# Optimization experiments

Hardware: AMD Instinct MI355X
Metric: run time of the kernel (lower is better)

The kernel has to match this reference:

```python
import jax, jax.numpy as jnp
import numpy as np

LAMBDA = 0.01  # sparsity_threshold
SCALE = 0.02
NUM_BLOCKS = 4


def setup_inputs() -> dict:
    key = jax.random.key(0)
    k1, k2, k3, k4, k5 = jax.random.split(key, 5)
    B, N, C = 8, 4096, 512
    bs = C // NUM_BLOCKS
    return {
        "x": jax.random.normal(k1, (B, N, C), dtype=jnp.float32),
        "w1": jax.random.normal(k2, (2, NUM_BLOCKS, bs, bs), dtype=jnp.float32) * SCALE,
        "w2": jax.random.normal(k3, (2, NUM_BLOCKS, bs, bs), dtype=jnp.float32) * SCALE,
        "b1": jax.random.normal(k4, (2, NUM_BLOCKS, bs), dtype=jnp.float32) * SCALE,
        "b2": jax.random.normal(k5, (2, NUM_BLOCKS, bs), dtype=jnp.float32) * SCALE,
        "H": 64,
        "W": 64,
    }


def _softshrink(v):
    return jnp.where(v > LAMBDA, v - LAMBDA, jnp.where(v < -LAMBDA, v + LAMBDA, jnp.zeros((), v.dtype)))


def reference(x, w1, w2, b1, b2, H, W):
    B, N, C = x.shape
    bs = C // NUM_BLOCKS
    xb = x.reshape(B, N, NUM_BLOCKS, bs)
    # FFT over (token, block) axes, ortho norm — faithful to torch fft2(dim=(1,2))
    xf = jnp.fft.fft2(xb, axes=(1, 2), norm="ortho")
    re, im = jnp.real(xf), jnp.imag(xf)

    mul = lambda a, w: jnp.einsum("tnbd,bdk->tnbk", a, w)  # block-diagonal matmul

    r1 = jax.nn.relu(mul(re, w1[0]) - mul(im, w1[1]) + b1[0])
    i1 = jax.nn.relu(mul(re, w1[1]) + mul(im, w1[0]) + b1[1])
    r2 = mul(r1, w2[0]) - mul(i1, w2[1]) + b2[0]
    i2 = mul(r1, w2[1]) + mul(i1, w2[0]) + b2[1]

    z = _softshrink(r2) + 1j * _softshrink(i2)
    out = jnp.real(jnp.fft.ifft2(z, axes=(1, 2), norm="ortho"))  # .to(float32) keeps real part
    return out.reshape(B, N, C).astype(jnp.float32)
```

## Files before the change

kernel.cpp:

```cpp
#include <hip/hip_runtime.h>
#include <math.h>

#define TWO_PI 6.283185307179586f

typedef __attribute__((ext_vector_type(8))) short bf16x8;
typedef __attribute__((ext_vector_type(4))) short bf16x4;
typedef __attribute__((ext_vector_type(4))) float f32x4;
typedef __attribute__((ext_vector_type(4))) _Float16 h16x4;
typedef __attribute__((ext_vector_type(8))) _Float16 h16x8;

__device__ __forceinline__ short f2bf(float f) {
    unsigned u = __float_as_uint(f);
    unsigned r = (u + 0x7FFFu + ((u >> 16) & 1u)) >> 16;
    return (short)r;
}
__device__ __forceinline__ float bf2f(short s) {
    return __uint_as_float(((unsigned)(unsigned short)s) << 16);
}

__device__ __forceinline__ int dr4(int s) {
    return ((s & 3) << 4) | (s & 12) | ((s >> 4) & 3);
}

__device__ __forceinline__ void cmulw(float& xr, float& xi, float wr, float wi) {
    const float tr = xr * wr - xi * wi;
    xi = xr * wi + xi * wr;
    xr = tr;
}

__device__ __forceinline__ f32x4 ld4bf(const char* Z, int off) {
    const bf16x4 v = *(const bf16x4*)(Z + off);
    f32x4 r;
    r[0] = bf2f(v[0]); r[1] = bf2f(v[1]); r[2] = bf2f(v[2]); r[3] = bf2f(v[3]);
    return r;
}
__device__ __forceinline__ void st4bf(char* Z, int off, f32x4 a) {
    bf16x4 v;
    v[0] = f2bf(a[0]); v[1] = f2bf(a[1]); v[2] = f2bf(a[2]); v[3] = f2bf(a[3]);
    *(bf16x4*)(Z + off) = v;
}

__device__ __forceinline__ int swzoff(int r, int cb) {
    return r * 256 + (cb ^ ((r & 7) << 4));
}

__device__ __forceinline__ void dif_stage_bf(char* Z, const float* wtr, const float* wti,
                                             int cb, int h, int s) {
    const int q  = 16 >> (2 * s);
    const int tw = 1 << (2 * s);
    const int j = h & (q - 1);
    const int g = (s == 0) ? 0 : (h >> (4 - 2 * s));
    const int i0 = g * (q << 2) + j;
    const int i1 = i0 + q, i2 = i1 + q, i3 = i2 + q;
    const int o0 = swzoff(i0, cb), o1 = swzoff(i1, cb);
    const int o2 = swzoff(i2, cb), o3 = swzoff(i3, cb);
    const f32x4 a0r = ld4bf(Z, o0), a0i = ld4bf(Z + 16384, o0);
    const f32x4 a1r = ld4bf(Z, o1), a1i = ld4bf(Z + 16384, o1);
    const f32x4 a2r = ld4bf(Z, o2), a2i = ld4bf(Z + 16384, o2);
    const f32x4 a3r = ld4bf(Z, o3), a3i = ld4bf(Z + 16384, o3);
    const int m = j * tw;
    const float w1r = wtr[m],     w1i = wti[m];
    const float w2r = wtr[2 * m], w2i = wti[2 * m];
    const float w3r = wtr[3 * m], w3i = wti[3 * m];
    f32x4 O0r, O0i, O1r, O1i, O2r, O2i, O3r, O3i;
#pragma unroll
    for (int e = 0; e < 4; ++e) {
        const float t0r = a0r[e] + a2r[e], t0i = a0i[e] + a2i[e];
        const float t2r = a0r[e] - a2r[e], t2i = a0i[e] - a2i[e];
        const float t1r = a1r[e] + a3r[e], t1i = a1i[e] + a3i[e];
        const float dr  = a1r[e] - a3r[e], di  = a1i[e] - a3i[e];
        const float t3r = di, t3i = -dr;
        O0r[e] = t0r + t1r;  O0i[e] = t0i + t1i;
        float y1r = t2r + t3r, y1i = t2i + t3i;
        float y2r = t0r - t1r, y2i = t0i - t1i;
        float y3r = t2r - t3r, y3i = t2i - t3i;
        if (m) {
            cmulw(y1r, y1i, w1r, w1i);
            cmulw(y2r, y2i, w2r, w2i);
            cmulw(y3r, y3i, w3r, w3i);
        }
        O1r[e] = y1r; O1i[e] = y1i;
        O2r[e] = y2r; O2i[e] = y2i;
        O3r[e] = y3r; O3i[e] = y3i;
    }
    st4bf(Z, o0, O0r);  st4bf(Z + 16384, o0, O0i);
    st4bf(Z, o1, O1r);  st4bf(Z + 16384, o1, O1i);
    st4bf(Z, o2, O2r);  st4bf(Z + 16384, o2, O2i);
    st4bf(Z, o3, O3r);  st4bf(Z + 16384, o3, O3i);
}

__device__ __forceinline__ void dit_stage_bf(char* Z, const float* wtr, const float* wti,
                                             int cb, int h, int s) {
    const int q  = 16 >> (2 * s);
    const int tw = 1 << (2 * s);
    const int j = h & (q - 1);
    const int g = (s == 0) ? 0 : (h >> (4 - 2 * s));
    const int i0 = g * (q << 2) + j;
    const int i1 = i0 + q, i2 = i1 + q, i3 = i2 + q;
    const int o0 = swzoff(i0, cb), o1 = swzoff(i1, cb);
    const int o2 = swzoff(i2, cb), o3 = swzoff(i3, cb);
    const f32x4 a0r = ld4bf(Z, o0), a0i = ld4bf(Z + 16384, o0);
    const f32x4 a1r = ld4bf(Z, o1), a1i = ld4bf(Z + 16384, o1);
    const f32x4 a2r = ld4bf(Z, o2), a2i = ld4bf(Z + 16384, o2);
    const f32x4 a3r = ld4bf(Z, o3), a3i = ld4bf(Z + 16384, o3);
    const int m = j * tw;
    const float w1r = wtr[m],     w1i = -wti[m];
    const float w2r = wtr[2 * m], w2i = -wti[2 * m];
    const float w3r = wtr[3 * m], w3i = -wti[3 * m];
    f32x4 O0r, O0i, O1r, O1i, O2r, O2i, O3r, O3i;
#pragma unroll
    for (int e = 0; e < 4; ++e) {
        float b1r = a1r[e], b1i = a1i[e];
        float b2r = a2r[e], b2i = a2i[e];
        float b3r = a3r[e], b3i = a3i[e];
        if (m) {
            cmulw(b1r, b1i, w1r, w1i);
            cmulw(b2r, b2i, w2r, w2i);
            cmulw(b3r, b3i, w3r, w3i);
        }
        const float u0r = a0r[e] + b2r, u0i = a0i[e] + b2i;
        const float u1r = a0r[e] - b2r, u1i = a0i[e] - b2i;
        const float u2r = b1r + b3r,    u2i = b1i + b3i;
        const float dr  = b1r - b3r,    di  = b1i - b3i;
        const float u3r = -di, u3i = dr;
        O0r[e] = u0r + u2r; O0i[e] = u0i + u2i;
        O1r[e] = u1r + u3r; O1i[e] = u1i + u3i;
        O2r[e] = u0r - u2r; O2i[e] = u0i - u2i;
        O3r[e] = u1r - u3r; O3i[e] = u1i - u3i;
    }
    st4bf(Z, o0, O0r);  st4bf(Z + 16384, o0, O0i);
    st4bf(Z, o1, O1r);  st4bf(Z + 16384, o1, O1i);
    st4bf(Z, o2, O2r);  st4bf(Z + 16384, o2, O2i);
    st4bf(Z, o3, O3r);  st4bf(Z + 16384, o3, O3i);
}

__device__ __forceinline__ void stage_ztile(const short* __restrict__ zre,
                                            const short* __restrict__ zim,
                                            char* Zbuf, int b, int dg, int ct,
                                            int wave, int lane) {
#pragma unroll
    for (int it = 0; it < 4; ++it) {
        const int q = wave * 256 + it * 64 + lane;
        const int p = q >> 10;
        const int r = q & 1023;
        const int slot = r >> 4;
        const int c = r & 15;
        const int c_log = c ^ (slot & 7);
        const int blk = c_log >> 2, cj = c_log & 3;
        const short* src = p ? zim : zre;
        const size_t g = ((size_t)(b * 4096 + dg * 64 + slot) * 512)
                       + (size_t)(blk * 128 + ct * 32 + cj * 8);
        unsigned* lp = (unsigned*)(Zbuf + (wave * 4096 + it * 1024));
        __builtin_amdgcn_global_load_lds((const unsigned*)(src + g), lp, 16, 0, 0);
    }
}

#define DECODE_BCT() \
    const int b  = blockIdx.x >> 8; \
    const int dg = (blockIdx.x >> 2) & 63; \
    const int ct = blockIdx.x & 3;

#define GADDR(slot, blk, f4) \
    (((size_t)(b * 4096 + (slot)) * 512) + (size_t)((blk) * 128 + ct * 32 + (f4) * 4))

#define GADDR8(slot, blk, e8) \
    (((size_t)(b * 4096 + (slot)) * 512) + (size_t)((blk) * 128 + ct * 32 + (e8) * 8))

#define SETUP_TABLE48() \
    if (tid < 48) { \
        float s_, c_; \
        sincosf(TWO_PI * (float)tid / 64.0f, &s_, &c_); \
        wre[tid] = c_; wim[tid] = -s_; \
    }

extern "C" __global__ void __launch_bounds__(512)
fft_fwd_a(const float* __restrict__ x, short* __restrict__ zre, short* __restrict__ zim) {
    __shared__ __align__(16) _Float16 Lre[64][136];
    __shared__ __align__(16) _Float16 Lim[64][136];
    __shared__ float wre[48], wim[48];
    __shared__ float twr[64], twi[64];
    const int tid = threadIdx.x;
    SETUP_TABLE48();
    DECODE_BCT();
    if (tid >= 64 && tid < 128) {
        const int s1 = tid - 64;
        float sn, cs;
        sincosf(-(TWO_PI / 4096.0f) * (float)(dg * dr4(s1)), &sn, &cs);
        twr[s1] = cs; twi[s1] = sn;
    }
    for (int idx = tid; idx < 2048; idx += 512) {
        const int n1 = idx >> 5, q = idx & 31, blk = q >> 3, f4 = q & 7;
        const int cl = blk * 32 + f4 * 4;
        const float4 v = *(const float4*)(x + GADDR(n1 * 64 + dg, blk, f4));
        h16x4 hv, hz;
        hv[0] = (_Float16)v.x; hv[1] = (_Float16)v.y;
        hv[2] = (_Float16)v.z; hv[3] = (_Float16)v.w;
        hz[0] = (_Float16)0.f; hz[1] = (_Float16)0.f;
        hz[2] = (_Float16)0.f; hz[3] = (_Float16)0.f;
        *(h16x4*)&Lre[n1][cl] = hv;
        *(h16x4*)&Lim[n1][cl] = hz;
    }
    {
        const int c4 = (tid & 31) * 4;
        const int h = tid >> 5;
#pragma unroll
        for (int s = 0; s < 3; ++s) {
            const int q  = 16 >> (2 * s);
            const int tw = 1 << (2 * s);
            __syncthreads();
            const int j = h & (q - 1);
            const int g = (s == 0) ? 0 : (h >> (4 - 2 * s));
            const int i0 = g * (q << 2) + j;
            const int i1 = i0 + q, i2 = i1 + q, i3 = i2 + q;
            const h16x4 A0r = *(const h16x4*)&Lre[i0][c4], A0i = *(const h16x4*)&Lim[i0][c4];
            const h16x4 A1r = *(const h16x4*)&Lre[i1][c4], A1i = *(const h16x4*)&Lim[i1][c4];
            const h16x4 A2r = *(const h16x4*)&Lre[i2][c4], A2i = *(const h16x4*)&Lim[i2][c4];
            const h16x4 A3r = *(const h16x4*)&Lre[i3][c4], A3i = *(const h16x4*)&Lim[i3][c4];
            const int m = j * tw;
            const float w1r = wre[m],     w1i = wim[m];
            const float w2r = wre[2 * m], w2i = wim[2 * m];
            const float w3r = wre[3 * m], w3i = wim[3 * m];
            h16x4 O0r, O0i, O1r, O1i, O2r, O2i, O3r, O3i;
#pragma unroll
            for (int e = 0; e < 4; ++e) {
                const float a0r = (float)A0r[e], a0i = (float)A0i[e];
                const float a1r = (float)A1r[e], a1i = (float)A1i[e];
                const float a2r = (float)A2r[e], a2i = (float)A2i[e];
                const float a3r = (float)A3r[e], a3i = (float)A3i[e];
                const float t0r = a0r + a2r, t0i = a0i + a2i;
                const float t2r = a0r - a2r, t2i = a0i - a2i;
                const float t1r = a1r + a3r, t1i = a1i + a3i;
                const float dr  = a1r - a3r, di  = a1i - a3i;
                const float t3r = di, t3i = -dr;
                O0r[e] = (_Float16)(t0r + t1r);  O0i[e] = (_Float16)(t0i + t1i);
                float y1r = t2r + t3r, y1i = t2i + t3i;
                float y2r = t0r - t1r, y2i = t0i - t1i;
                float y3r = t2r - t3r, y3i = t2i - t3i;
                if (m) {
                    cmulw(y1r, y1i, w1r, w1i);
                    cmulw(y2r, y2i, w2r, w2i);
                    cmulw(y3r, y3i, w3r, w3i);
                }
                O1r[e] = (_Float16)y1r; O1i[e] = (_Float16)y1i;
                O2r[e] = (_Float16)y2r; O2i[e] = (_Float16)y2i;
                O3r[e] = (_Float16)y3r; O3i[e] = (_Float16)y3i;
            }
            *(h16x4*)&Lre[i0][c4] = O0r;  *(h16x4*)&Lim[i0][c4] = O0i;
            *(h16x4*)&Lre[i1][c4] = O1r;  *(h16x4*)&Lim[i1][c4] = O1i;
            *(h16x4*)&Lre[i2][c4] = O2r;  *(h16x4*)&Lim[i2][c4] = O2i;
            *(h16x4*)&Lre[i3][c4] = O3r;  *(h16x4*)&Lim[i3][c4] = O3i;
        }
        __syncthreads();
    }
    for (int idx = tid; idx < 2048; idx += 512) {
        const int s1 = idx >> 5, q = idx & 31, blk = q >> 3, f4 = q & 7;
        const int cl = blk * 32 + f4 * 4;
        const float cs = twr[s1], sn = twi[s1];
        const h16x4 hr = *(const h16x4*)&Lre[s1][cl];
        const h16x4 hi = *(const h16x4*)&Lim[s1][cl];
        bf16x4 pr, pi;
#pragma unroll
        for (int i = 0; i < 4; ++i) {
            const float vr = (float)hr[i], vi = (float)hi[i];
            pr[i] = f2bf(vr * cs - vi * sn);
            pi[i] = f2bf(vr * sn + vi * cs);
        }
        const size_t g = GADDR(s1 * 64 + dg, blk, f4);
        *(bf16x4*)(zre + g) = pr;
        *(bf16x4*)(zim + g) = pi;
    }
}

extern "C" __global__ void __launch_bounds__(512)
fft_fwd_b(short* __restrict__ zre, short* __restrict__ zim) {
    __shared__ __align__(16) char Zs[2][32768];
    __shared__ float wre[48], wim[48];
    const int tid = threadIdx.x;
    SETUP_TABLE48();
    const int bh = blockIdx.x >> 8;
    const int dg = (blockIdx.x >> 2) & 63;
    const int ct = blockIdx.x & 3;
    const int wave = tid >> 6, lane = tid & 63;
    const int cb = (tid & 31) * 8;
    const int h  = tid >> 5;

    stage_ztile(zre, zim, Zs[0], bh * 4, dg, ct, wave, lane);

    for (int t = 0; t < 4; ++t) {
        __syncthreads();
        if (t + 1 < 4)
            stage_ztile(zre, zim, Zs[(t + 1) & 1], bh * 4 + t + 1, dg, ct, wave, lane);

        char* Z = Zs[t & 1];
        dif_stage_bf(Z, wre, wim, cb, h, 0);
        __syncthreads();
        dif_stage_bf(Z, wre, wim, cb, h, 1);
        __syncthreads();
        dif_stage_bf(Z, wre, wim, cb, h, 2);
        __syncthreads();

        {
            const int slot = tid >> 3, jg4 = tid & 7;
            const int jb = jg4 * 8;
            f32x4 r[4], m[4];
#pragma unroll
            for (int b4 = 0; b4 < 4; ++b4) {
                const int off = swzoff(slot, b4 * 64 + jb);
                r[b4] = ld4bf(Z, off);
                m[b4] = ld4bf(Z + 16384, off);
            }
            const float sc = 1.0f / 128.0f;
            f32x4 yr[4], ym[4];
#pragma unroll
            for (int e = 0; e < 4; ++e) {
                const float r0 = r[0][e], r1 = r[1][e], r2 = r[2][e], r3 = r[3][e];
                const float m0 = m[0][e], m1 = m[1][e], m2 = m[2][e], m3 = m[3][e];
                yr[0][e] = (r0 + r1 + r2 + r3) * sc;  ym[0][e] = (m0 + m1 + m2 + m3) * sc;
                yr[1][e] = (r0 + m1 - r2 - m3) * sc;  ym[1][e] = (m0 - r1 - m2 + r3) * sc;
                yr[2][e] = (r0 - r1 + r2 - r3) * sc;  ym[2][e] = (m0 - m1 + m2 - m3) * sc;
                yr[3][e] = (r0 - m1 - r2 + m3) * sc;  ym[3][e] = (m0 + r1 - m2 - r3) * sc;
            }
#pragma unroll
            for (int b4 = 0; b4 < 4; ++b4) {
                const int off = swzoff(slot, b4 * 64 + jb);
                st4bf(Z, off, yr[b4]);
                st4bf(Z + 16384, off, ym[b4]);
            }
        }
        __syncthreads();

        const int b = bh * 4 + t;
#pragma unroll
        for (int kq = 0; kq < 4; ++kq) {
            const int q = wave * 256 + kq * 64 + lane;
            const int p = q >> 10;
            const int r2 = q & 1023;
            const int slot = r2 >> 4;
            const int c = r2 & 15;
            const int c_log = c ^ (slot & 7);
            const int blk = c_log >> 2, cj = c_log & 3;
            const bf16x8 v = *(const bf16x8*)(Z + q * 16);
            short* dst = p ? zim : zre;
            const size_t g = ((size_t)(b * 4096 + dg * 64 + slot) * 512)
                           + (size_t)(blk * 128 + ct * 32 + cj * 8);
            *(bf16x8*)(dst + g) = v;
        }
    }
}

extern "C" __global__ void __launch_bounds__(512)
fft_inv_a(short* __restrict__ zre, short* __restrict__ zim) {
    __shared__ __align__(16) char Zs[2][32768];
    __shared__ float wre[48], wim[48];
    __shared__ float twr[64], twi[64];
    const int tid = threadIdx.x;
    SETUP_TABLE48();
    const int bh = blockIdx.x >> 8;
    const int dg = (blockIdx.x >> 2) & 63;
    const int ct = blockIdx.x & 3;
    if (tid >= 64 && tid < 128) {
        const int n2 = tid - 64;
        float sn, cs;
        sincosf((TWO_PI / 4096.0f) * (float)(n2 * dr4(dg)), &sn, &cs);
        twr[n2] = cs; twi[n2] = sn;
    }
    const int wave = tid >> 6, lane = tid & 63;
    const int cb = (tid & 31) * 8;
    const int h  = tid >> 5;

    stage_ztile(zre, zim, Zs[0], bh * 4, dg, ct, wave, lane);

    for (int t = 0; t < 4; ++t) {
        __syncthreads();
        if (t + 1 < 4)
            stage_ztile(zre, zim, Zs[(t + 1) & 1], bh * 4 + t + 1, dg, ct, wave, lane);

        char* Z = Zs[t & 1];

        {
            const int slot = tid >> 3, jg4 = tid & 7;
            const int jb = jg4 * 8;
            f32x4 r[4], m[4];
#pragma unroll
            for (int b4 = 0; b4 < 4; ++b4) {
                const int off = swzoff(slot, b4 * 64 + jb);
                r[b4] = ld4bf(Z, off);
                m[b4] = ld4bf(Z + 16384, off);
            }
            const float sc = 1.0f / 128.0f;
            f32x4 yr[4], ym[4];
#pragma unroll
            for (int e = 0; e < 4; ++e) {
                const float r0 = r[0][e], r1 = r[1][e], r2 = r[2][e], r3 = r[3][e];
                const float m0 = m[0][e], m1 = m[1][e], m2 = m[2][e], m3 = m[3][e];
                yr[0][e] = (r0 + r1 + r2 + r3) * sc;  ym[0][e] = (m0 + m1 + m2 + m3) * sc;
                yr[1][e] = (r0 - m1 - r2 + m3) * sc;  ym[1][e] = (m0 + r1 - m2 - r3) * sc;
                yr[2][e] = (r0 - r1 + r2 - r3) * sc;  ym[2][e] = (m0 - m1 + m2 - m3) * sc;
                yr[3][e] = (r0 + m1 - r2 - m3) * sc;  ym[3][e] = (m0 - r1 - m2 + r3) * sc;
            }
#pragma unroll
            for (int b4 = 0; b4 < 4; ++b4) {
                const int off = swzoff(slot, b4 * 64 + jb);
                st4bf(Z, off, yr[b4]);
                st4bf(Z + 16384, off, ym[b4]);
            }
        }
        __syncthreads();
        dit_stage_bf(Z, wre, wim, cb, h, 2);
        __syncthreads();
        dit_stage_bf(Z, wre, wim, cb, h, 1);
        __syncthreads();
        dit_stage_bf(Z, wre, wim, cb, h, 0);
        __syncthreads();

        const int b = bh * 4 + t;
#pragma unroll
        for (int k = 0; k < 2; ++k) {
            const int idx = tid + k * 512;
            const int slot = idx >> 4;
            const int c = idx & 15;
            const int c_log = c ^ (slot & 7);
            const int blk = c_log >> 2, cj = c_log & 3;
            const bf16x8 vr = *(const bf16x8*)(Z + slot * 256 + c * 16);
            const bf16x8 vi = *(const bf16x8*)(Z + 16384 + slot * 256 + c * 16);
            const float cs = twr[slot], sn = twi[slot];
            bf16x8 pr, pi;
#pragma unroll
            for (int i = 0; i < 8; ++i) {
                const float ar = bf2f(vr[i]), ai = bf2f(vi[i]);
                pr[i] = f2bf(ar * cs - ai * sn);
                pi[i] = f2bf(ar * sn + ai * cs);
            }
            const size_t g = ((size_t)(b * 4096 + dg * 64 + slot) * 512)
                           + (size_t)(blk * 128 + ct * 32 + cj * 8);
            *(bf16x8*)(zre + g) = pr;
            *(bf16x8*)(zim + g) = pi;
        }
    }
}

extern "C" __global__ void __launch_bounds__(512)
fft_inv_b(const short* __restrict__ zre, const short* __restrict__ zim,
          float* __restrict__ out) {
    __shared__ __align__(16) _Float16 Lre[64][136];
    __shared__ __align__(16) _Float16 Lim[64][136];
    __shared__ float wre[48], wim[48];
    const int tid = threadIdx.x;
    SETUP_TABLE48();
    DECODE_BCT();
    for (int idx = tid; idx < 1024; idx += 512) {
        const int s1 = idx >> 4, q = idx & 15, blk = q >> 2, e8 = q & 3;
        const int cl = blk * 32 + e8 * 8;
        const size_t g = GADDR8(s1 * 64 + dg, blk, e8);
        const bf16x8 vr = *(const bf16x8*)(zre + g);
        const bf16x8 vi = *(const bf16x8*)(zim + g);
        h16x8 hr, hi;
#pragma unroll
        for (int i = 0; i < 8; ++i) {
            hr[i] = (_Float16)bf2f(vr[i]);
            hi[i] = (_Float16)bf2f(vi[i]);
        }
        *(h16x8*)&Lre[s1][cl] = hr;
        *(h16x8*)&Lim[s1][cl] = hi;
    }
    {
        const int c4 = (tid & 31) * 4;
        const int h = tid >> 5;
#pragma unroll
        for (int s = 2; s >= 0; --s) {
            const int q  = 16 >> (2 * s);
            const int tw = 1 << (2 * s);
            __syncthreads();
            const int j = h & (q - 1);
            const int g = (s == 0) ? 0 : (h >> (4 - 2 * s));
            const int i0 = g * (q << 2) + j;
            const int i1 = i0 + q, i2 = i1 + q, i3 = i2 + q;
            const h16x4 A0r = *(const h16x4*)&Lre[i0][c4], A0i = *(const h16x4*)&Lim[i0][c4];
            const h16x4 A1r = *(const h16x4*)&Lre[i1][c4], A1i = *(const h16x4*)&Lim[i1][c4];
            const h16x4 A2r = *(const h16x4*)&Lre[i2][c4], A2i = *(const h16x4*)&Lim[i2][c4];
            const h16x4 A3r = *(const h16x4*)&Lre[i3][c4], A3i = *(const h16x4*)&Lim[i3][c4];
            const int m = j * tw;
            const float w1r = wre[m],     w1i = -wim[m];
            const float w2r = wre[2 * m], w2i = -wim[2 * m];
            const float w3r = wre[3 * m], w3i = -wim[3 * m];
            h16x4 O0r, O0i, O1r, O1i, O2r, O2i, O3r, O3i;
#pragma unroll
            for (int e = 0; e < 4; ++e) {
                float b1r = (float)A1r[e], b1i = (float)A1i[e];
                float b2r = (float)A2r[e], b2i = (float)A2i[e];
                float b3r = (float)A3r[e], b3i = (float)A3i[e];
                if (m) {
                    cmulw(b1r, b1i, w1r, w1i);
                    cmulw(b2r, b2i, w2r, w2i);
                    cmulw(b3r, b3i, w3r, w3i);
                }
                const float a0r = (float)A0r[e], a0i = (float)A0i[e];
                const float u0r = a0r + b2r, u0i = a0i + b2i;
                const float u1r = a0r - b2r, u1i = a0i - b2i;
                const float u2r = b1r + b3r, u2i = b1i + b3i;
                const float dr  = b1r - b3r, di  = b1i - b3i;
                const float u3r = -di, u3i = dr;
                O0r[e] = (_Float16)(u0r + u2r); O0i[e] = (_Float16)(u0i + u2i);
                O1r[e] = (_Float16)(u1r + u3r); O1i[e] = (_Float16)(u1i + u3i);
                O2r[e] = (_Float16)(u0r - u2r); O2i[e] = (_Float16)(u0i - u2i);
                O3r[e] = (_Float16)(u1r - u3r); O3i[e] = (_Float16)(u1i - u3i);
            }
            *(h16x4*)&Lre[i0][c4] = O0r;  *(h16x4*)&Lim[i0][c4] = O0i;
            *(h16x4*)&Lre[i1][c4] = O1r;  *(h16x4*)&Lim[i1][c4] = O1i;
            *(h16x4*)&Lre[i2][c4] = O2r;  *(h16x4*)&Lim[i2][c4] = O2i;
            *(h16x4*)&Lre[i3][c4] = O3r;  *(h16x4*)&Lim[i3][c4] = O3i;
        }
        __syncthreads();
    }
    for (int idx = tid; idx < 2048; idx += 512) {
        const int n1 = idx >> 5, q = idx & 31, blk = q >> 3, f4 = q & 7;
        const int cl = blk * 32 + f4 * 4;
        const h16x4 hr = *(const h16x4*)&Lre[n1][cl];
        float4 o;
        o.x = (float)hr[0]; o.y = (float)hr[1];
        o.z = (float)hr[2]; o.w = (float)hr[3];
        *(float4*)(out + GADDR(n1 * 64 + dg, blk, f4)) = o;
    }
}

extern "C" __global__ void __launch_bounds__(256)
wprep(const float* __restrict__ w1, const float* __restrict__ w2,
      short* __restrict__ wb) {
    const int i4  = blockIdx.x * 256 + threadIdx.x;
    const int k0  = (i4 & 63) * 4;
    const int n   = (i4 >> 6) & 255;
    const int blk = (i4 >> 14) & 3;
    const int L   = i4 >> 16;
    const float* w = L ? w2 : w1;
    bf16x4 pv;
#pragma unroll
    for (int j = 0; j < 4; ++j) {
        const int k = k0 + j;
        float v;
        if (k < 128) {
            v = (n < 128) ? w[blk * 16384 + k * 128 + n]
                          : w[65536 + blk * 16384 + k * 128 + (n - 128)];
        } else {
            v = (n < 128) ? -w[65536 + blk * 16384 + (k - 128) * 128 + n]
                          :  w[blk * 16384 + (k - 128) * 128 + (n - 128)];
        }
        pv[j] = f2bf(v);
    }
    *(bf16x4*)(wb + (size_t)i4 * 4) = pv;
}

#define MITER 4

__device__ __forceinline__ void stage_tile(const short* __restrict__ zre,
                                           const short* __restrict__ zim,
                                           char* Abuf, int rowbase, int blk,
                                           int wave, int lane) {
#pragma unroll
    for (int it = 0; it < 4; ++it) {
        const int chunk = wave * 256 + it * 64 + lane;
        const int row   = chunk >> 5;
        const unsigned kbyte = ((unsigned)((chunk & 31) << 4)) ^ ((unsigned)((row & 7) << 4));
        const int k0 = (int)(kbyte >> 1);
        const short* src = (k0 < 128) ? zre : zim;
        const size_t g = (size_t)(rowbase + row) * 512 + blk * 128 + (k0 & 127);
        unsigned* lp = (unsigned*)(Abuf + (wave * 4096 + it * 1024));
        __builtin_amdgcn_global_load_lds((const unsigned*)(src + g), lp, 16, 0, 0);
    }
}

template<int LAYER>
__global__ void __launch_bounds__(512)
mlp_mfma(short* __restrict__ zre, short* __restrict__ zim,
         const short* __restrict__ wb, const float* __restrict__ bias) {
    __shared__ __align__(16) char As[2][64 * 256 * 2];

    const int blk  = blockIdx.y;
    const int tid  = threadIdx.x;
    const int wave = tid >> 6;
    const int lane = tid & 63;
    const int lrow = lane & 15;
    const int lk   = lane >> 4;

    bf16x8 Bf[2][8];
#pragma unroll
    for (int nt = 0; nt < 2; ++nt) {
        const int n = wave * 32 + nt * 16 + lrow;
#pragma unroll
        for (int ks = 0; ks < 8; ++ks) {
            Bf[nt][ks] = *(const bf16x8*)(wb + ((size_t)(blk * 256 + n) * 256 + ks * 32 + lk * 8));
        }
    }

    float bv[2];
#pragma unroll
    for (int nt = 0; nt < 2; ++nt) {
        const int n = wave * 32 + nt * 16 + lrow;
        bv[nt] = (n < 128) ? bias[blk * 128 + n] : bias[512 + blk * 128 + (n - 128)];
    }

    stage_tile(zre, zim, As[0], blockIdx.x * MITER * 64, blk, wave, lane);

    for (int t = 0; t < MITER; ++t) {
        __syncthreads();

        if (t + 1 < MITER)
            stage_tile(zre, zim, As[(t + 1) & 1],
                       (blockIdx.x * MITER + t + 1) * 64, blk, wave, lane);

        const char* Ab = As[t & 1];
        const int rowbase = (blockIdx.x * MITER + t) * 64;

        f32x4 acc[4][2];
#pragma unroll
        for (int mt = 0; mt < 4; ++mt)
#pragma unroll
            for (int nt = 0; nt < 2; ++nt)
                acc[mt][nt] = (f32x4){0.f, 0.f, 0.f, 0.f};

#pragma unroll
        for (int ks = 0; ks < 8; ++ks) {
            bf16x8 af[4];
#pragma unroll
            for (int mt = 0; mt < 4; ++mt) {
                const int row = mt * 16 + lrow;
                const int k0  = ks * 32 + lk * 8;
                const unsigned byteoff =
                    ((unsigned)(row * 512 + k0 * 2)) ^ ((unsigned)((row & 7) << 4));
                af[mt] = *(const bf16x8*)(Ab + byteoff);
            }
#pragma unroll
            for (int mt = 0; mt < 4; ++mt)
#pragma unroll
                for (int nt = 0; nt < 2; ++nt)
                    acc[mt][nt] = __builtin_amdgcn_mfma_f32_16x16x32_bf16(
                        af[mt], Bf[nt][ks], acc[mt][nt], 0, 0, 0);
        }

#pragma unroll
        for (int nt = 0; nt < 2; ++nt) {
            const int n = wave * 32 + nt * 16 + lrow;
            short* dst = (n < 128) ? zre : zim;
            const int col = blk * 128 + (n & 127);
#pragma unroll
            for (int mt = 0; mt < 4; ++mt) {
#pragma unroll
                for (int r = 0; r < 4; ++r) {
                    const int row = rowbase + mt * 16 + lk * 4 + r;
                    float v = acc[mt][nt][r] + bv[nt];
                    if (LAYER == 1) {
                        v = fmaxf(v, 0.0f);
                    } else {
                        v = (v > 0.01f) ? v - 0.01f : ((v < -0.01f) ? v + 0.01f : 0.0f);
                    }
                    dst[(size_t)row * 512 + col] = f2bf(v);
                }
            }
        }
    }
}

extern "C" void kernel_launch(void* const* d_in, const int* in_sizes, int n_in,
                              void* d_out, int out_size, void* d_ws, size_t ws_size,
                              hipStream_t stream) {
    const float* x  = (const float*)d_in[0];
    const float* w1 = (const float*)d_in[1];
    const float* w2 = (const float*)d_in[2];
    const float* b1 = (const float*)d_in[3];
    const float* b2 = (const float*)d_in[4];

    float* out = (float*)d_out;
    short* zre = (short*)d_ws;
    short* zim = zre + 16777216;
    short* wb  = (short*)d_out;
    const size_t WB_L = 4ull * 256 * 256;

    wprep<<<512, 256, 0, stream>>>(w1, w2, wb);

    fft_fwd_a<<<2048, 512, 0, stream>>>(x, zre, zim);
    fft_fwd_b<<<512, 512, 0, stream>>>(zre, zim);

    mlp_mfma<1><<<dim3(32768 / (64 * MITER), 4), 512, 0, stream>>>(zre, zim, wb, b1);
    mlp_mfma<2><<<dim3(32768 / (64 * MITER), 4), 512, 0, stream>>>(zre, zim, wb + WB_L, b2);

    fft_inv_a<<<512, 512, 0, stream>>>(zre, zim);
    fft_inv_b<<<2048, 512, 0, stream>>>(zre, zim, out);
}
```

Before: 235.3 us.

## Move 4-point block DFT into token-FFT kernels and halve per-block batch loop

The radix-4 DFT over the channel-block axis moves out of fft_fwd_b and fft_inv_a. It now runs in registers at the end of fft_fwd_a (after the twiddle) and at the start of fft_inv_b, which removes one LDS read/write pass and a barrier from each of the heavy 64x64 kernels. fft_fwd_b and fft_inv_a drop their double-buffered LDS staging for a single buffer and process two batches per block instead of four, with twice as many blocks launched. Results are read into registers before the next tile is staged. The radix-4 64-point butterflies are factored into shared templates. The trade-off is less load/compute overlap inside each block, in exchange for lower LDS use and more blocks in flight.

```diff
diff --git a/kernel.cpp b/kernel.cpp
--- a/kernel.cpp
+++ b/kernel.cpp
@@ -163,15 +163,117 @@
 #define GADDR(slot, blk, f4) \
     (((size_t)(b * 4096 + (slot)) * 512) + (size_t)((blk) * 128 + ct * 32 + (f4) * 4))
 
-#define GADDR8(slot, blk, e8) \
-    (((size_t)(b * 4096 + (slot)) * 512) + (size_t)((blk) * 128 + ct * 32 + (e8) * 8))
-
 #define SETUP_TABLE48() \
     if (tid < 48) { \
         float s_, c_; \
         sincosf(TWO_PI * (float)tid / 64.0f, &s_, &c_); \
         wre[tid] = c_; wim[tid] = -s_; \
     }
+
+template<int W>
+__device__ __forceinline__ void fft64_dif4v(_Float16 (*Lre)[W], _Float16 (*Lim)[W],
+                                            const float* wtr, const float* wti,
+                                            int c4, int h) {
+#pragma unroll
+    for (int s = 0; s < 3; ++s) {
+        const int q  = 16 >> (2 * s);
+        const int tw = 1 << (2 * s);
+        __syncthreads();
+        const int j = h & (q - 1);
+        const int g = (s == 0) ? 0 : (h >> (4 - 2 * s));
+        const int i0 = g * (q << 2) + j;
+        const int i1 = i0 + q, i2 = i1 + q, i3 = i2 + q;
+        const h16x4 A0r = *(const h16x4*)&Lre[i0][c4], A0i = *(const h16x4*)&Lim[i0][c4];
+        const h16x4 A1r = *(const h16x4*)&Lre[i1][c4], A1i = *(const h16x4*)&Lim[i1][c4];
+        const h16x4 A2r = *(const h16x4*)&Lre[i2][c4], A2i = *(const h16x4*)&Lim[i2][c4];
+        const h16x4 A3r = *(const h16x4*)&Lre[i3][c4], A3i = *(const h16x4*)&Lim[i3][c4];
+        const int m = j * tw;
+        const float w1r = wtr[m],     w1i = wti[m];
+        const float w2r = wtr[2 * m], w2i = wti[2 * m];
+        const float w3r = wtr[3 * m], w3i = wti[3 * m];
+        h16x4 O0r, O0i, O1r, O1i, O2r, O2i, O3r, O3i;
+#pragma unroll
+        for (int e = 0; e < 4; ++e) {
+            const float a0r = (float)A0r[e], a0i = (float)A0i[e];
+            const float a1r = (float)A1r[e], a1i = (float)A1i[e];
+            const float a2r = (float)A2r[e], a2i = (float)A2i[e];
+            const float a3r = (float)A3r[e], a3i = (float)A3i[e];
+            const float t0r = a0r + a2r, t0i = a0i + a2i;
+            const float t2r = a0r - a2r, t2i = a0i - a2i;
+            const float t1r = a1r + a3r, t1i = a1i + a3i;
+            const float dr  = a1r - a3r, di  = a1i - a3i;
+            const float t3r = di, t3i = -dr;
+            O0r[e] = (_Float16)(t0r + t1r);  O0i[e] = (_Float16)(t0i + t1i);
+            float y1r = t2r + t3r, y1i = t2i + t3i;
+            float y2r = t0r - t1r, y2i = t0i - t1i;
+            float y3r = t2r - t3r, y3i = t2i - t3i;
+            if (m) {
+                cmulw(y1r, y1i, w1r, w1i);
+                cmulw(y2r, y2i, w2r, w2i);
+                cmulw(y3r, y3i, w3r, w3i);
+            }
+            O1r[e] = (_Float16)y1r; O1i[e] = (_Float16)y1i;
+            O2r[e] = (_Float16)y2r; O2i[e] = (_Float16)y2i;
+            O3r[e] = (_Float16)y3r; O3i[e] = (_Float16)y3i;
+        }
+        *(h16x4*)&Lre[i0][c4] = O0r;  *(h16x4*)&Lim[i0][c4] = O0i;
+        *(h16x4*)&Lre[i1][c4] = O1r;  *(h16x4*)&Lim[i1][c4] = O1i;
+        *(h16x4*)&Lre[i2][c4] = O2r;  *(h16x4*)&Lim[i2][c4] = O2i;
+        *(h16x4*)&Lre[i3][c4] = O3r;  *(h16x4*)&Lim[i3][c4] = O3i;
+    }
+    __syncthreads();
+}
+
+template<int W>
+__device__ __forceinline__ void fft64_dit4v(_Float16 (*Lre)[W], _Float16 (*Lim)[W],
+                                            const float* wtr, const float* wti,
+                                            int c4, int h) {
+#pragma unroll
+    for (int s = 2; s >= 0; --s) {
+        const int q  = 16 >> (2 * s);
+        const int tw = 1 << (2 * s);
+        __syncthreads();
+        const int j = h & (q - 1);
+        const int g = (s == 0) ? 0 : (h >> (4 - 2 * s));
+        const int i0 = g * (q << 2) + j;
+        const int i1 = i0 + q, i2 = i1 + q, i3 = i2 + q;
+        const h16x4 A0r = *(const h16x4*)&Lre[i0][c4], A0i = *(const h16x4*)&Lim[i0][c4];
+        const h16x4 A1r = *(const h16x4*)&Lre[i1][c4], A1i = *(const h16x4*)&Lim[i1][c4];
+        const h16x4 A2r = *(const h16x4*)&Lre[i2][c4], A2i = *(const h16x4*)&Lim[i2][c4];
+        const h16x4 A3r = *(const h16x4*)&Lre[i3][c4], A3i = *(const h16x4*)&Lim[i3][c4];
+        const int m = j * tw;
+        const float w1r = wtr[m],     w1i = -wti[m];
+        const float w2r = wtr[2 * m], w2i = -wti[2 * m];
+        const float w3r = wtr[3 * m], w3i = -wti[3 * m];
+        h16x4 O0r, O0i, O1r, O1i, O2r, O2i, O3r, O3i;
+#pragma unroll
+        for (int e = 0; e < 4; ++e) {
+            float b1r = (float)A1r[e], b1i = (float)A1i[e];
+            float b2r = (float)A2r[e], b2i = (float)A2i[e];
+            float b3r = (float)A3r[e], b3i = (float)A3i[e];
+            if (m) {
+                cmulw(b1r, b1i, w1r, w1i);
+                cmulw(b2r, b2i, w2r, w2i);
+                cmulw(b3r, b3i, w3r, w3i);
+            }
+            const float a0r = (float)A0r[e], a0i = (float)A0i[e];
+            const float u0r = a0r + b2r, u0i = a0i + b2i;
+            const float u1r = a0r - b2r, u1i = a0i - b2i;
+            const float u2r = b1r + b3r, u2i = b1i + b3i;
+            const float dr  = b1r - b3r, di  = b1i - b3i;
+            const float u3r = -di, u3i = dr;
+            O0r[e] = (_Float16)(u0r + u2r); O0i[e] = (_Float16)(u0i + u2i);
+            O1r[e] = (_Float16)(u1r + u3r); O1i[e] = (_Float16)(u1i + u3i);
+            O2r[e] = (_Float16)(u0r - u2r); O2i[e] = (_Float16)(u0i - u2i);
+            O3r[e] = (_Float16)(u1r - u3r); O3i[e] = (_Float16)(u1i - u3i);
+        }
+        *(h16x4*)&Lre[i0][c4] = O0r;  *(h16x4*)&Lim[i0][c4] = O0i;
+        *(h16x4*)&Lre[i1][c4] = O1r;  *(h16x4*)&Lim[i1][c4] = O1i;
+        *(h16x4*)&Lre[i2][c4] = O2r;  *(h16x4*)&Lim[i2][c4] = O2i;
+        *(h16x4*)&Lre[i3][c4] = O3r;  *(h16x4*)&Lim[i3][c4] = O3i;
+    }
+    __syncthreads();
+}
 
 extern "C" __global__ void __launch_bounds__(512)
 fft_fwd_a(const float* __restrict__ x, short* __restrict__ zre, short* __restrict__ zim) {
@@ -200,80 +302,52 @@
         *(h16x4*)&Lre[n1][cl] = hv;
         *(h16x4*)&Lim[n1][cl] = hz;
     }
+    fft64_dif4v<136>(Lre, Lim, wre, wim, (tid & 31) * 4, tid >> 5);
     {
-        const int c4 = (tid & 31) * 4;
-        const int h = tid >> 5;
-#pragma unroll
-        for (int s = 0; s < 3; ++s) {
-            const int q  = 16 >> (2 * s);
-            const int tw = 1 << (2 * s);
-            __syncthreads();
-            const int j = h & (q - 1);
-            const int g = (s == 0) ? 0 : (h >> (4 - 2 * s));
-            const int i0 = g * (q << 2) + j;
-            const int i1 = i0 + q, i2 = i1 + q, i3 = i2 + q;
-            const h16x4 A0r = *(const h16x4*)&Lre[i0][c4], A0i = *(const h16x4*)&Lim[i0][c4];
-            const h16x4 A1r = *(const h16x4*)&Lre[i1][c4], A1i = *(const h16x4*)&Lim[i1][c4];
-            const h16x4 A2r = *(const h16x4*)&Lre[i2][c4], A2i = *(const h16x4*)&Lim[i2][c4];
-            const h16x4 A3r = *(const h16x4*)&Lre[i3][c4], A3i = *(const h16x4*)&Lim[i3][c4];
-            const int m = j * tw;
-            const float w1r = wre[m],     w1i = wim[m];
-            const float w2r = wre[2 * m], w2i = wim[2 * m];
-            const float w3r = wre[3 * m], w3i = wim[3 * m];
-            h16x4 O0r, O0i, O1r, O1i, O2r, O2i, O3r, O3i;
+        const int s1 = tid >> 3, f4 = tid & 7;
+        const float cs = twr[s1], sn = twi[s1];
+        f32x4 r[4], m[4];
+#pragma unroll
+        for (int blk = 0; blk < 4; ++blk) {
+            const int cl = blk * 32 + f4 * 4;
+            const h16x4 hr = *(const h16x4*)&Lre[s1][cl];
+            const h16x4 hi = *(const h16x4*)&Lim[s1][cl];
 #pragma unroll
             for (int e = 0; e < 4; ++e) {
-                const float a0r = (float)A0r[e], a0i = (float)A0i[e];
-                const float a1r = (float)A1r[e], a1i = (float)A1i[e];
-                const float a2r = (float)A2r[e], a2i = (float)A2i[e];
-                const float a3r = (float)A3r[e], a3i = (float)A3i[e];
-                const float t0r = a0r + a2r, t0i = a0i + a2i;
-                const float t2r = a0r - a2r, t2i = a0i - a2i;
-                const float t1r = a1r + a3r, t1i = a1i + a3i;
-                const float dr  = a1r - a3r, di  = a1i - a3i;
-                const float t3r = di, t3i = -dr;
-                O0r[e] = (_Float16)(t0r + t1r);  O0i[e] = (_Float16)(t0i + t1i);
-                float y1r = t2r + t3r, y1i = t2i + t3i;
-                float y2r = t0r - t1r, y2i = t0i - t1i;
-                float y3r = t2r - t3r, y3i = t2i - t3i;
-                if (m) {
-                    cmulw(y1r, y1i, w1r, w1i);
-                    cmulw(y2r, y2i, w2r, w2i);
-                    cmulw(y3r, y3i, w3r, w3i);
-                }
-                O1r[e] = (_Float16)y1r; O1i[e] = (_Float16)y1i;
-                O2r[e] = (_Float16)y2r; O2i[e] = (_Float16)y2i;
-                O3r[e] = (_Float16)y3r; O3i[e] = (_Float16)y3i;
-            }
-            *(h16x4*)&Lre[i0][c4] = O0r;  *(h16x4*)&Lim[i0][c4] = O0i;
-            *(h16x4*)&Lre[i1][c4] = O1r;  *(h16x4*)&Lim[i1][c4] = O1i;
-            *(h16x4*)&Lre[i2][c4] = O2r;  *(h16x4*)&Lim[i2][c4] = O2i;
-            *(h16x4*)&Lre[i3][c4] = O3r;  *(h16x4*)&Lim[i3][c4] = O3i;
-        }
-        __syncthreads();
-    }
-    for (int idx = tid; idx < 2048; idx += 512) {
-        const int s1 = idx >> 5, q = idx & 31, blk = q >> 3, f4 = q & 7;
-        const int cl = blk * 32 + f4 * 4;
-        const float cs = twr[s1], sn = twi[s1];
-        const h16x4 hr = *(const h16x4*)&Lre[s1][cl];
-        const h16x4 hi = *(const h16x4*)&Lim[s1][cl];
-        bf16x4 pr, pi;
-#pragma unroll
-        for (int i = 0; i < 4; ++i) {
-            const float vr = (float)hr[i], vi = (float)hi[i];
-            pr[i] = f2bf(vr * cs - vi * sn);
-            pi[i] = f2bf(vr * sn + vi * cs);
-        }
-        const size_t g = GADDR(s1 * 64 + dg, blk, f4);
-        *(bf16x4*)(zre + g) = pr;
-        *(bf16x4*)(zim + g) = pi;
+                const float vr = (float)hr[e], vi = (float)hi[e];
+                r[blk][e] = vr * cs - vi * sn;
+                m[blk][e] = vr * sn + vi * cs;
+            }
+        }
+        const float sc = 1.0f / 128.0f;
+        f32x4 yr[4], ym[4];
+#pragma unroll
+        for (int e = 0; e < 4; ++e) {
+            const float r0 = r[0][e], r1 = r[1][e], r2 = r[2][e], r3 = r[3][e];
+            const float m0 = m[0][e], m1 = m[1][e], m2 = m[2][e], m3 = m[3][e];
+            yr[0][e] = (r0 + r1 + r2 + r3) * sc;  ym[0][e] = (m0 + m1 + m2 + m3) * sc;
+            yr[1][e] = (r0 + m1 - r2 - m3) * sc;  ym[1][e] = (m0 - r1 - m2 + r3) * sc;
+            yr[2][e] = (r0 - r1 + r2 - r3) * sc;  ym[2][e] = (m0 - m1 + m2 - m3) * sc;
+            yr[3][e] = (r0 - m1 - r2 + m3) * sc;  ym[3][e] = (m0 + r1 - m2 - r3) * sc;
+        }
+#pragma unroll
+        for (int blk = 0; blk < 4; ++blk) {
+            bf16x4 pr, pi;
+#pragma unroll
+            for (int e = 0; e < 4; ++e) {
+                pr[e] = f2bf(yr[blk][e]);
+                pi[e] = f2bf(ym[blk][e]);
+            }
+            const size_t g = GADDR(s1 * 64 + dg, blk, f4);
+            *(bf16x4*)(zre + g) = pr;
+            *(bf16x4*)(zim + g) = pi;
+        }
     }
 }
 
 extern "C" __global__ void __launch_bounds__(512)
 fft_fwd_b(short* __restrict__ zre, short* __restrict__ zim) {
-    __shared__ __align__(16) char Zs[2][32768];
+    __shared__ __align__(16) char Zs[32768];
     __shared__ float wre[48], wim[48];
     const int tid = threadIdx.x;
     SETUP_TABLE48();
@@ -284,52 +358,26 @@
     const int cb = (tid & 31) * 8;
     const int h  = tid >> 5;
 
-    stage_ztile(zre, zim, Zs[0], bh * 4, dg, ct, wave, lane);
-
-    for (int t = 0; t < 4; ++t) {
-        __syncthreads();
-        if (t + 1 < 4)
-            stage_ztile(zre, zim, Zs[(t + 1) & 1], bh * 4 + t + 1, dg, ct, wave, lane);
-
-        char* Z = Zs[t & 1];
-        dif_stage_bf(Z, wre, wim, cb, h, 0);
-        __syncthreads();
-        dif_stage_bf(Z, wre, wim, cb, h, 1);
-        __syncthreads();
-        dif_stage_bf(Z, wre, wim, cb, h, 2);
-        __syncthreads();
-
-        {
-            const int slot = tid >> 3, jg4 = tid & 7;
-            const int jb = jg4 * 8;
-            f32x4 r[4], m[4];
-#pragma unroll
-            for (int b4 = 0; b4 < 4; ++b4) {
-                const int off = swzoff(slot, b4 * 64 + jb);
-                r[b4] = ld4bf(Z, off);
-                m[b4] = ld4bf(Z + 16384, off);
-            }
-            const float sc = 1.0f / 128.0f;
-            f32x4 yr[4], ym[4];
-#pragma unroll
-            for (int e = 0; e < 4; ++e) {
-                const float r0 = r[0][e], r1 = r[1][e], r2 = r[2][e], r3 = r[3][e];
-                const float m0 = m[0][e], m1 = m[1][e], m2 = m[2][e], m3 = m[3][e];
-                yr[0][e] = (r0 + r1 + r2 + r3) * sc;  ym[0][e] = (m0 + m1 + m2 + m3) * sc;
-                yr[1][e] = (r0 + m1 - r2 - m3) * sc;  ym[1][e] = (m0 - r1 - m2 + r3) * sc;
-                yr[2][e] = (r0 - r1 + r2 - r3) * sc;  ym[2][e] = (m0 - m1 + m2 - m3) * sc;
-                yr[3][e] = (r0 - m1 - r2 + m3) * sc;  ym[3][e] = (m0 + r1 - m2 - r3) * sc;
-            }
-#pragma unroll
-            for (int b4 = 0; b4 < 4; ++b4) {
-                const int off = swzoff(slot, b4 * 64 + jb);
-                st4bf(Z, off, yr[b4]);
-                st4bf(Z + 16384, off, ym[b4]);
-            }
-        }
-        __syncthreads();
-
-        const int b = bh * 4 + t;
+    stage_ztile(zre, zim, Zs, bh * 2, dg, ct, wave, lane);
+
+    for (int t = 0; t < 2; ++t) {
+        __syncthreads();
+        dif_stage_bf(Zs, wre, wim, cb, h, 0);
+        __syncthreads();
+        dif_stage_bf(Zs, wre, wim, cb, h, 1);
+        __syncthreads();
+        dif_stage_bf(Zs, wre, wim, cb, h, 2);
+        __syncthreads();
+        bf16x8 vout[4];
+#pragma unroll
+        for (int kq = 0; kq < 4; ++kq) {
+            const int q = wave * 256 + kq * 64 + lane;
+            vout[kq] = *(const bf16x8*)(Zs + q * 16);
+        }
+        __syncthreads();
+        if (t + 1 < 2)
+            stage_ztile(zre, zim, Zs, bh * 2 + t + 1, dg, ct, wave, lane);
+        const int b = bh * 2 + t;
 #pragma unroll
         for (int kq = 0; kq < 4; ++kq) {
             const int q = wave * 256 + kq * 64 + lane;
@@ -339,18 +387,17 @@
             const int c = r2 & 15;
             const int c_log = c ^ (slot & 7);
             const int blk = c_log >> 2, cj = c_log & 3;
-            const bf16x8 v = *(const bf16x8*)(Z + q * 16);
             short* dst = p ? zim : zre;
             const size_t g = ((size_t)(b * 4096 + dg * 64 + slot) * 512)
                            + (size_t)(blk * 128 + ct * 32 + cj * 8);
-            *(bf16x8*)(dst + g) = v;
+            *(bf16x8*)(dst + g) = vout[kq];
         }
     }
 }
 
 extern "C" __global__ void __launch_bounds__(512)
 fft_inv_a(short* __restrict__ zre, short* __restrict__ zim) {
-    __shared__ __align__(16) char Zs[2][32768];
+    __shared__ __align__(16) char Zs[32768];
     __shared__ float wre[48], wim[48];
     __shared__ float twr[64], twi[64];
     const int tid = threadIdx.x;
@@ -368,52 +415,36 @@
     const int cb = (tid & 31) * 8;
     const int h  = tid >> 5;
 
-    stage_ztile(zre, zim, Zs[0], bh * 4, dg, ct, wave, lane);
-
-    for (int t = 0; t < 4; ++t) {
-        __syncthreads();
-        if (t + 1 < 4)
-            stage_ztile(zre, zim, Zs[(t + 1) & 1], bh * 4 + t + 1, dg, ct, wave, lane);
-
-        char* Z = Zs[t & 1];
-
-        {
-            const int slot = tid >> 3, jg4 = tid & 7;
-            const int jb = jg4 * 8;
-            f32x4 r[4], m[4];
-#pragma unroll
-            for (int b4 = 0; b4 < 4; ++b4) {
-                const int off = swzoff(slot, b4 * 64 + jb);
-                r[b4] = ld4bf(Z, off);
-                m[b4] = ld4bf(Z + 16384, off);
-            }
-            const float sc = 1.0f / 128.0f;
-            f32x4 yr[4], ym[4];
-#pragma unroll
-            for (int e = 0; e < 4; ++e) {
-                const float r0 = r[0][e], r1 = r[1][e], r2 = r[2][e], r3 = r[3][e];
-                const float m0 = m[0][e], m1 = m[1][e], m2 = m[2][e], m3 = m[3][e];
-                yr[0][e] = (r0 + r1 + r2 + r3) * sc;  ym[0][e] = (m0 + m1 + m2 + m3) * sc;
-                yr[1][e] = (r0 - m1 - r2 + m3) * sc;  ym[1][e] = (m0 + r1 - m2 - r3) * sc;
-                yr[2][e] = (r0 - r1 + r2 - r3) * sc;  ym[2][e] = (m0 - m1 + m2 - m3) * sc;
-                yr[3][e] = (r0 + m1 - r2 - m3) * sc;  ym[3][e] = (m0 - r1 - m2 + r3) * sc;
-            }
-#pragma unroll
-            for (int b4 = 0; b4 < 4; ++b4) {
-                const int off = swzoff(slot, b4 * 64 + jb);
-                st4bf(Z, off, yr[b4]);
-                st4bf(Z + 16384, off, ym[b4]);
-            }
-        }
-        __syncthreads();
-        dit_stage_bf(Z, wre, wim, cb, h, 2);
-        __syncthreads();
-        dit_stage_bf(Z, wre, wim, cb, h, 1);
-        __syncthreads();
-        dit_stage_bf(Z, wre, wim, cb, h, 0);
-        __syncthreads();
-
-        const int b = bh * 4 + t;
+    stage_ztile(zre, zim, Zs, bh * 2, dg, ct, wave, lane);
+
+    for (int t = 0; t < 2; ++t) {
+        __syncthreads();
+        dit_stage_bf(Zs, wre, wim, cb, h, 2);
+        __syncthreads();
+        dit_stage_bf(Zs, wre, wim, cb, h, 1);
+        __syncthreads();
+        dit_stage_bf(Zs, wre, wim, cb, h, 0);
+        __syncthreads();
+        bf16x8 pr[2], pi[2];
+#pragma unroll
+        for (int k = 0; k < 2; ++k) {
+            const int idx = tid + k * 512;
+            const int slot = idx >> 4;
+            const int c = idx & 15;
+            const bf16x8 vr = *(const bf16x8*)(Zs + slot * 256 + c * 16);
+            const bf16x8 vi = *(const bf16x8*)(Zs + 16384 + slot * 256 + c * 16);
+            const float cs = twr[slot], sn = twi[slot];
+#pragma unroll
+            for (int i = 0; i < 8; ++i) {
+                const float ar = bf2f(vr[i]), ai = bf2f(vi[i]);
+                pr[k][i] = f2bf(ar * cs - ai * sn);
+                pi[k][i] = f2bf(ar * sn + ai * cs);
+            }
+        }
+        __syncthreads();
+        if (t + 1 < 2)
+            stage_ztile(zre, zim, Zs, bh * 2 + t + 1, dg, ct, wave, lane);
+        const int b = bh * 2 + t;
 #pragma unroll
         for (int k = 0; k < 2; ++k) {
             const int idx = tid + k * 512;
@@ -421,20 +452,10 @@
             const int c = idx & 15;
             const int c_log = c ^ (slot & 7);
             const int blk = c_log >> 2, cj = c_log & 3;
-            const bf16x8 vr = *(const bf16x8*)(Z + slot * 256 + c * 16);
-            const bf16x8 vi = *(const bf16x8*)(Z + 16384 + slot * 256 + c * 16);
-            const float cs = twr[slot], sn = twi[slot];
-            bf16x8 pr, pi;
-#pragma unroll
-            for (int i = 0; i < 8; ++i) {
-                const float ar = bf2f(vr[i]), ai = bf2f(vi[i]);
-                pr[i] = f2bf(ar * cs - ai * sn);
-                pi[i] = f2bf(ar * sn + ai * cs);
-            }
             const size_t g = ((size_t)(b * 4096 + dg * 64 + slot) * 512)
                            + (size_t)(blk * 128 + ct * 32 + cj * 8);
-            *(bf16x8*)(zre + g) = pr;
-            *(bf16x8*)(zim + g) = pi;
+            *(bf16x8*)(zre + g) = pr[k];
+            *(bf16x8*)(zim + g) = pi[k];
         }
     }
 }
@@ -448,70 +469,45 @@
     const int tid = threadIdx.x;
     SETUP_TABLE48();
     DECODE_BCT();
-    for (int idx = tid; idx < 1024; idx += 512) {
-        const int s1 = idx >> 4, q = idx & 15, blk = q >> 2, e8 = q & 3;
-        const int cl = blk * 32 + e8 * 8;
-        const size_t g = GADDR8(s1 * 64 + dg, blk, e8);
-        const bf16x8 vr = *(const bf16x8*)(zre + g);
-        const bf16x8 vi = *(const bf16x8*)(zim + g);
-        h16x8 hr, hi;
-#pragma unroll
-        for (int i = 0; i < 8; ++i) {
-            hr[i] = (_Float16)bf2f(vr[i]);
-            hi[i] = (_Float16)bf2f(vi[i]);
-        }
-        *(h16x8*)&Lre[s1][cl] = hr;
-        *(h16x8*)&Lim[s1][cl] = hi;
-    }
     {
-        const int c4 = (tid & 31) * 4;
-        const int h = tid >> 5;
-#pragma unroll
-        for (int s = 2; s >= 0; --s) {
-            const int q  = 16 >> (2 * s);
-            const int tw = 1 << (2 * s);
-            __syncthreads();
-            const int j = h & (q - 1);
-            const int g = (s == 0) ? 0 : (h >> (4 - 2 * s));
-            const int i0 = g * (q << 2) + j;
-            const int i1 = i0 + q, i2 = i1 + q, i3 = i2 + q;
-            const h16x4 A0r = *(const h16x4*)&Lre[i0][c4], A0i = *(const h16x4*)&Lim[i0][c4];
-            const h16x4 A1r = *(const h16x4*)&Lre[i1][c4], A1i = *(const h16x4*)&Lim[i1][c4];
-            const h16x4 A2r = *(const h16x4*)&Lre[i2][c4], A2i = *(const h16x4*)&Lim[i2][c4];
-            const h16x4 A3r = *(const h16x4*)&Lre[i3][c4], A3i = *(const h16x4*)&Lim[i3][c4];
-            const int m = j * tw;
-            const float w1r = wre[m],     w1i = -wim[m];
-            const float w2r = wre[2 * m], w2i = -wim[2 * m];
-            const float w3r = wre[3 * m], w3i = -wim[3 * m];
-            h16x4 O0r, O0i, O1r, O1i, O2r, O2i, O3r, O3i;
+        const int s1 = tid >> 3, f4 = tid & 7;
+        f32x4 r[4], m[4];
+#pragma unroll
+        for (int blk = 0; blk < 4; ++blk) {
+            const size_t g = GADDR(s1 * 64 + dg, blk, f4);
+            const bf16x4 vr = *(const bf16x4*)(zre + g);
+            const bf16x4 vi = *(const bf16x4*)(zim + g);
 #pragma unroll
             for (int e = 0; e < 4; ++e) {
-                float b1r = (float)A1r[e], b1i = (float)A1i[e];
-                float b2r = (float)A2r[e], b2i = (float)A2i[e];
-                float b3r = (float)A3r[e], b3i = (float)A3i[e];
-                if (m) {
-                    cmulw(b1r, b1i, w1r, w1i);
-                    cmulw(b2r, b2i, w2r, w2i);
-                    cmulw(b3r, b3i, w3r, w3i);
-                }
-                const float a0r = (float)A0r[e], a0i = (float)A0i[e];
-                const float u0r = a0r + b2r, u0i = a0i + b2i;
-                const float u1r = a0r - b2r, u1i = a0i - b2i;
-                const float u2r = b1r + b3r, u2i = b1i + b3i;
-                const float dr  = b1r - b3r, di  = b1i - b3i;
-                const float u3r = -di, u3i = dr;
-                O0r[e] = (_Float16)(u0r + u2r); O0i[e] = (_Float16)(u0i + u2i);
-                O1r[e] = (_Float16)(u1r + u3r); O1i[e] = (_Float16)(u1i + u3i);
-                O2r[e] = (_Float16)(u0r - u2r); O2i[e] = (_Float16)(u0i - u2i);
-                O3r[e] = (_Float16)(u1r - u3r); O3i[e] = (_Float16)(u1i - u3i);
-            }
-            *(h16x4*)&Lre[i0][c4] = O0r;  *(h16x4*)&Lim[i0][c4] = O0i;
-            *(h16x4*)&Lre[i1][c4] = O1r;  *(h16x4*)&Lim[i1][c4] = O1i;
-            *(h16x4*)&Lre[i2][c4] = O2r;  *(h16x4*)&Lim[i2][c4] = O2i;
-            *(h16x4*)&Lre[i3][c4] = O3r;  *(h16x4*)&Lim[i3][c4] = O3i;
-        }
-        __syncthreads();
-    }
+                r[blk][e] = bf2f(vr[e]);
+                m[blk][e] = bf2f(vi[e]);
+            }
+        }
+        const float sc = 1.0f / 128.0f;
+        f32x4 yr[4], ym[4];
+#pragma unroll
+        for (int e = 0; e < 4; ++e) {
+            const float r0 = r[0][e], r1 = r[1][e], r2 = r[2][e], r3 = r[3][e];
+            const float m0 = m[0][e], m1 = m[1][e], m2 = m[2][e], m3 = m[3][e];
+            yr[0][e] = (r0 + r1 + r2 + r3) * sc;  ym[0][e] = (m0 + m1 + m2 + m3) * sc;
+            yr[1][e] = (r0 - m1 - r2 + m3) * sc;  ym[1][e] = (m0 + r1 - m2 - r3) * sc;
+            yr[2][e] = (r0 - r1 + r2 - r3) * sc;  ym[2][e] = (m0 - m1 + m2 - m3) * sc;
+            yr[3][e] = (r0 + m1 - r2 - m3) * sc;  ym[3][e] = (m0 - r1 - m2 + r3) * sc;
+        }
+#pragma unroll
+        for (int blk = 0; blk < 4; ++blk) {
+            const int cl = blk * 32 + f4 * 4;
+            h16x4 hr, hi;
+#pragma unroll
+            for (int e = 0; e < 4; ++e) {
+                hr[e] = (_Float16)yr[blk][e];
+                hi[e] = (_Float16)ym[blk][e];
+            }
+            *(h16x4*)&Lre[s1][cl] = hr;
+            *(h16x4*)&Lim[s1][cl] = hi;
+        }
+    }
+    fft64_dit4v<136>(Lre, Lim, wre, wim, (tid & 31) * 4, tid >> 5);
     for (int idx = tid; idx < 2048; idx += 512) {
         const int n1 = idx >> 5, q = idx & 31, blk = q >> 3, f4 = q & 7;
         const int cl = blk * 32 + f4 * 4;
@@ -677,11 +673,11 @@
     wprep<<<512, 256, 0, stream>>>(w1, w2, wb);
 
     fft_fwd_a<<<2048, 512, 0, stream>>>(x, zre, zim);
-    fft_fwd_b<<<512, 512, 0, stream>>>(zre, zim);
+    fft_fwd_b<<<1024, 512, 0, stream>>>(zre, zim);
 
     mlp_mfma<1><<<dim3(32768 / (64 * MITER), 4), 512, 0, stream>>>(zre, zim, wb, b1);
     mlp_mfma<2><<<dim3(32768 / (64 * MITER), 4), 512, 0, stream>>>(zre, zim, wb + WB_L, b2);
 
-    fft_inv_a<<<512, 512, 0, stream>>>(zre, zim);
+    fft_inv_a<<<1024, 512, 0, stream>>>(zre, zim);
     fft_inv_b<<<2048, 512, 0, stream>>>(zre, zim, out);
 }
```

Measured after the change: 222.5 us. -5.4%, faster.
